# Optimization experiments

Measured on AMD Instinct MI355X. Metric: run time of the kernel, lower is better.

Reference implementation:

```python
import jax, jax.numpy as jnp
import numpy as np

PS = 32    # base patch size
SUB = 16   # subdivided patch size produced by sigmoid_round for up-weighted patches


def _sigmoid_round_np(x):
    # mirrors torch: round(32*sigmoid(x-24) + 16*(1-sigmoid(x-24)))
    s = 1.0 / (1.0 + np.exp(-(x - 24.0)))
    return np.round(32.0 * s + 16.0 * (1.0 - s)).astype(np.int64)


def _build_importance(P):
    # deterministic importance weights: even patches slightly above the mean
    # (-> adaptive size 16, subdivided), odd patches below (-> size 32, kept).
    avg = 1.0 / P
    a = avg * (2.0 ** (1.0 / 12.0)) * 1.001
    b = 2.0 * avg - a
    iw = np.empty(P, np.float64)
    iw[0::2] = a
    iw[1::2] = b
    return iw


def _build_token_index(P, G):
    # Reproduces the torch module's per-patch structural decision at trace time
    # (numpy on deterministic constants -> static shapes, jit-safe).
    iw = _build_importance(P)
    avg = iw.mean()
    sizes = _sigmoid_round_np(PS * (avg ** 12) / (iw ** 12))
    tok = []
    for i in range(P):
        r, c = i // G, i % G
        if 7 < sizes[i] < PS:  # subdivided into (PS/SUB)^2 = 4 sub-patches, row-major
            for dr in range(PS // SUB):
                for dc in range(PS // SUB):
                    tok.append(G * G + (2 * r + dr) * (2 * G) + (2 * c + dc))
        else:                   # full 32x32 patch token
            tok.append(r * G + c)
    return np.asarray(tok, np.int32)


def setup_inputs() -> dict:
    key = jax.random.key(0)
    k1, k2, k3 = jax.random.split(key, 3)
    B, C, H, E = 32, 3, 512, 768
    x = jax.random.normal(k1, (B, C, H, H), jnp.float32)
    patch_weight = jax.random.normal(k2, (E, C, PS, PS), jnp.float32) * 0.02
    patch_bias = jax.random.normal(k3, (E,), jnp.float32) * 0.02
    P = (H // PS) ** 2
    importance_w = jnp.asarray(_build_importance(P), jnp.float32)
    return {"x": x, "importance_w": importance_w, "patch_weight": patch_weight,
            "patch_bias": patch_bias, "num_patches": P}


def reference(x, importance_w, patch_weight, patch_bias, num_patches):
    B, C, H, _ = x.shape
    E = patch_weight.shape[0]
    G = H // PS            # 32x32 patch grid side
    kd = PS // SUB         # kernel divisor = 2
    tok_idx = _build_token_index(num_patches, G)  # static gather structure

    # full-size patches: stride-PS conv on each 32x32 tile == one GEMM
    # x tiles: (b, c, r, i, q, j) with row = r*PS+i, col = q*PS+j
    full = jnp.einsum('bcriqj,ecij->brqe',
                      x.reshape(B, C, G, PS, G, PS), patch_weight) + patch_bias

    # averaged 16x16 kernel: view(E,C,kd,kd,SUB,SUB).mean(dim=2).mean(dim=2)
    w_sub = patch_weight.reshape(E, C, kd, kd, SUB, SUB).mean(axis=(2, 3))
    sub = jnp.einsum('bcriqj,ecij->brqe',
                     x.reshape(B, C, kd * G, SUB, kd * G, SUB), w_sub) + patch_bias

    # token pool: [full 32-tiles (G*G), then all 16-tiles ((2G)^2)]; gather in
    # original patch order with subdivided patches expanded in place.
    pool = jnp.concatenate([full.reshape(B, G * G, E),
                            sub.reshape(B, (kd * G) ** 2, E)], axis=1)
    return pool[:, tok_idx, :]
```

## Files before the change

### kernel.cpp

```cpp
#include <hip/hip_runtime.h>
#include <stdint.h>


typedef __attribute__((ext_vector_type(8))) short bf16x8;
typedef __attribute__((ext_vector_type(8))) unsigned short ushort8;
typedef __attribute__((ext_vector_type(4))) float f32x4;

__device__ __forceinline__ unsigned short f2bf(float f) {
  union { float f; unsigned u; } v; v.f = f;
  return (unsigned short)((v.u + 0x7fffu + ((v.u >> 16) & 1u)) >> 16);
}
__device__ __forceinline__ float bf2f(unsigned short h) {
  union { unsigned u; float f; } v; v.u = ((unsigned)h) << 16; return v.f;
}

__global__ __launch_bounds__(256) void prep_w(const float* __restrict__ pw,
                                              unsigned short* __restrict__ Wf,
                                              unsigned short* __restrict__ Ws) {
  int bid = blockIdx.x, t = threadIdx.x;
  if (bid < 2304) {
    int g = bid * 256 + t;
    float4 v = ((const float4*)pw)[g];
    ((ushort4*)Wf)[g] = make_ushort4(f2bf(v.x), f2bf(v.y), f2bf(v.z), f2bf(v.w));
  } else {
    int g = (bid - 2304) * 256 + t;
    int e = g / 192;
    int rem = g - e * 192;
    int cc = rem >> 6, r2 = rem & 63, s = r2 >> 2, t4 = r2 & 3;
    const float* base = pw + ((size_t)((e * 3 + cc) * 32 + (s >> 1)) * 32
                              + 16 * (s & 1) + 4 * t4);
    float4 q0 = *(const float4*)(base);
    float4 q1 = *(const float4*)(base + 8 * 32);
    float4 q2 = *(const float4*)(base + 16 * 32);
    float4 q3 = *(const float4*)(base + 24 * 32);
    ((ushort4*)Ws)[g] = make_ushort4(
        f2bf(0.25f * (q0.x + q1.x + q2.x + q3.x)),
        f2bf(0.25f * (q0.y + q1.y + q2.y + q3.y)),
        f2bf(0.25f * (q0.z + q1.z + q2.z + q3.z)),
        f2bf(0.25f * (q0.w + q1.w + q2.w + q3.w)));
  }
}

__global__ __launch_bounds__(256) void gemm_fused(
    const float* __restrict__ x,
    const unsigned short* __restrict__ Wf, const unsigned short* __restrict__ Ws,
    const float* __restrict__ bias, unsigned short* __restrict__ Pf,
    float* __restrict__ out) {
  __shared__ unsigned short Asm[128 * 64];
  __shared__ unsigned short Bsm[128 * 64];

  int bid = (blockIdx.x & 7) * 192 + (blockIdx.x >> 3);

  const unsigned short* Bbase;
  int rsB, bm, bn, kofs, which, kc = 0;
  int ccsh, iish, iimask, jjmask;
  if (bid < 768) {
    which = 0;
    int grp = bid / 6; bn = bid - grp * 6;
    bm = grp >> 2; kc = grp & 3;
    rsB = 3072; kofs = kc * 768;
    Bbase = Wf;
    ccsh = 10; iish = 5; iimask = 31; jjmask = 31;
  } else {
    which = 1;
    int id = bid - 768;
    bm = id / 6; bn = id - bm * 6;
    rsB = 768; kofs = 0;
    Bbase = Ws;
    ccsh = 8; iish = 4; iimask = 15; jjmask = 15;
  }

  int t = threadIdx.x;
  int lane = t & 63;
  int wv = t >> 6, wr = wv >> 1, wc = wv & 1;
  int lr = lane & 15, lk = lane >> 4;

  int kbase = kofs + (t & 7) * 8;
  int abase[4];
#pragma unroll
  for (int is = 0; is < 4; ++is) {
    int m = bm * 128 + (t >> 3) + is * 32;
    int b, r, cp, extra;
    if (which == 0) {
      b = m >> 7; int p = m & 127; int i = 2 * p + 1;
      r = i >> 4; cp = i & 15; extra = 0;
    } else {
      b = m >> 9; int q = m & 511; int p = q >> 2, s = q & 3;
      int dr = s >> 1, dc = s & 1; int i = 2 * p;
      r = i >> 4; cp = i & 15; extra = dr * 8192 + dc * 16;
    }
    abase[is] = b * 786432 + r * 16384 + cp * 32 + extra;
  }
  const unsigned short* b_src = Bbase + (size_t)(bn * 128 + (t >> 3)) * rsB
                                + (t & 7) * 8 + kofs;
  unsigned short* as_dst = &Asm[t * 8];
  unsigned short* bs_dst = &Bsm[t * 8];

  f32x4 acc[4][4];
#pragma unroll
  for (int mm = 0; mm < 4; ++mm)
#pragma unroll
    for (int nn = 0; nn < 4; ++nn) acc[mm][nn] = (f32x4){0.f, 0.f, 0.f, 0.f};

  for (int k0 = 0; k0 < 768; k0 += 64) {
#pragma unroll
    for (int is = 0; is < 4; ++is)
      __builtin_amdgcn_global_load_lds(
          (const __attribute__((address_space(1))) void*)(b_src + (size_t)is * 32 * rsB + k0),
          (__attribute__((address_space(3))) void*)(bs_dst + is * 2048), 16, 0, 0);
    float4 va[4][2];
    int k = kbase + k0;
    int koff = (k >> ccsh) * 262144 + ((k >> iish) & iimask) * 512 + (k & jjmask);
#pragma unroll
    for (int is = 0; is < 4; ++is) {
      const float4* s4 = (const float4*)(x + abase[is] + koff);
      va[is][0] = s4[0]; va[is][1] = s4[1];
    }
#pragma unroll
    for (int is = 0; is < 4; ++is) {
      ushort8 v;
      v[0] = f2bf(va[is][0].x); v[1] = f2bf(va[is][0].y);
      v[2] = f2bf(va[is][0].z); v[3] = f2bf(va[is][0].w);
      v[4] = f2bf(va[is][1].x); v[5] = f2bf(va[is][1].y);
      v[6] = f2bf(va[is][1].z); v[7] = f2bf(va[is][1].w);
      *(ushort8*)(as_dst + is * 2048) = v;
    }
    __syncthreads();
#pragma unroll
    for (int kk = 0; kk < 64; kk += 32) {
      bf16x8 af[4], bf[4];
#pragma unroll
      for (int mm = 0; mm < 4; ++mm)
        af[mm] = *(const bf16x8*)&Asm[(wr * 64 + mm * 16 + lr) * 64 + kk + lk * 8];
#pragma unroll
      for (int nn = 0; nn < 4; ++nn)
        bf[nn] = *(const bf16x8*)&Bsm[(wc * 64 + nn * 16 + lr) * 64 + kk + lk * 8];
#pragma unroll
      for (int mm = 0; mm < 4; ++mm)
#pragma unroll
        for (int nn = 0; nn < 4; ++nn)
          acc[mm][nn] = __builtin_amdgcn_mfma_f32_16x16x32_bf16(af[mm], bf[nn], acc[mm][nn], 0, 0, 0);
    }
    __syncthreads();
  }

#pragma unroll
  for (int mm = 0; mm < 4; ++mm) {
    int trow = wr * 64 + mm * 16 + lk * 4;
#pragma unroll
    for (int reg = 0; reg < 4; ++reg) {
      int grow = bm * 128 + trow + reg;
      if (which == 0) {
        unsigned short* pdst = Pf + ((size_t)(kc * 4096 + grow)) * 768;
#pragma unroll
        for (int nn = 0; nn < 4; ++nn) {
          int gcol = bn * 128 + wc * 64 + nn * 16 + lr;
          pdst[gcol] = f2bf(acc[mm][nn][reg]);
        }
      } else {
        int b = grow >> 9, tt2 = grow & 511, p = tt2 >> 2, s = tt2 & 3;
        size_t obase = (size_t)(b * 640 + 5 * p + s) * 768;
#pragma unroll
        for (int nn = 0; nn < 4; ++nn) {
          int gcol = bn * 128 + wc * 64 + nn * 16 + lr;
          out[obase + gcol] = acc[mm][nn][reg] + bias[gcol];
        }
      }
    }
  }
}

__global__ __launch_bounds__(256) void reduce_full(
    const unsigned short* __restrict__ Pf, const float* __restrict__ bias,
    float* __restrict__ out) {
  int q = blockIdx.x * 256 + threadIdx.x;
  int m = q / 192, c4 = q - m * 192;
  float4 sacc = ((const float4*)bias)[c4];
#pragma unroll
  for (int kc = 0; kc < 4; ++kc) {
    ushort4 u = ((const ushort4*)(Pf + ((size_t)(kc * 4096 + m)) * 768))[c4];
    sacc.x += bf2f(u.x); sacc.y += bf2f(u.y);
    sacc.z += bf2f(u.z); sacc.w += bf2f(u.w);
  }
  int b = m >> 7, p = m & 127;
  size_t obase = (size_t)(b * 640 + 5 * p + 4) * 768;
  ((float4*)(out + obase))[c4] = sacc;
}

extern "C" void kernel_launch(void* const* d_in, const int* in_sizes, int n_in,
                              void* d_out, int out_size, void* d_ws, size_t ws_size,
                              hipStream_t stream) {
  const float* x  = (const float*)d_in[0];
  const float* pw = (const float*)d_in[2];
  const float* pb = (const float*)d_in[3];
  float* out = (float*)d_out;

  unsigned short* Wf = (unsigned short*)d_ws;
  unsigned short* Ws = Wf + 2359296;
  unsigned short* Pf = Ws + 589824;

  prep_w<<<2880, 256, 0, stream>>>(pw, Wf, Ws);
  gemm_fused<<<1536, 256, 0, stream>>>(x, Wf, Ws, pb, Pf, out);
  reduce_full<<<3072, 256, 0, stream>>>(Pf, pb, out);
}
```

Before: 244.6 us.

## Double-buffer GEMM LDS tiles with BK=32, padded A and swizzled B

```diff
diff --git a/kernel.cpp b/kernel.cpp
--- a/kernel.cpp
+++ b/kernel.cpp
@@ -41,13 +41,13 @@
   }
 }
 
-__global__ __launch_bounds__(256) void gemm_fused(
+__global__ __launch_bounds__(256, 3) void gemm_fused(
     const float* __restrict__ x,
     const unsigned short* __restrict__ Wf, const unsigned short* __restrict__ Ws,
     const float* __restrict__ bias, unsigned short* __restrict__ Pf,
     float* __restrict__ out) {
-  __shared__ unsigned short Asm[128 * 64];
-  __shared__ unsigned short Bsm[128 * 64];
+  __shared__ unsigned short Asm[2][128 * 40];
+  __shared__ unsigned short Bsm[2][128 * 32];
 
   int bid = (blockIdx.x & 7) * 192 + (blockIdx.x >> 3);
 
@@ -75,26 +75,27 @@
   int wv = t >> 6, wr = wv >> 1, wc = wv & 1;
   int lr = lane & 15, lk = lane >> 4;
 
-  int kbase = kofs + (t & 7) * 8;
-  int abase[4];
-#pragma unroll
-  for (int is = 0; is < 4; ++is) {
-    int m = bm * 128 + (t >> 3) + is * 32;
+  int abase[2], kA[2], awr[2];
+  const unsigned short* bsrc[2];
+#pragma unroll
+  for (int is = 0; is < 2; ++is) {
+    int slot = t + 256 * is;
+    int row = slot >> 2, ch = slot & 3;
+    int m = bm * 128 + row;
     int b, r, cp, extra;
     if (which == 0) {
       b = m >> 7; int p = m & 127; int i = 2 * p + 1;
       r = i >> 4; cp = i & 15; extra = 0;
     } else {
-      b = m >> 9; int q = m & 511; int p = q >> 2, s = q & 3;
-      int dr = s >> 1, dc = s & 1; int i = 2 * p;
-      r = i >> 4; cp = i & 15; extra = dr * 8192 + dc * 16;
+      b = m >> 9; int q = m & 511; int p = q >> 2, sq = q & 3;
+      int i = 2 * p; r = i >> 4; cp = i & 15;
+      extra = (sq >> 1) * 8192 + (sq & 1) * 16;
     }
     abase[is] = b * 786432 + r * 16384 + cp * 32 + extra;
-  }
-  const unsigned short* b_src = Bbase + (size_t)(bn * 128 + (t >> 3)) * rsB
-                                + (t & 7) * 8 + kofs;
-  unsigned short* as_dst = &Asm[t * 8];
-  unsigned short* bs_dst = &Bsm[t * 8];
+    kA[is] = kofs + ch * 8;
+    awr[is] = row * 40 + ch * 8;
+    bsrc[is] = Bbase + (size_t)(bn * 128 + row) * rsB + kofs + ((ch ^ (row & 3)) * 8);
+  }
 
   f32x4 acc[4][4];
 #pragma unroll
@@ -102,44 +103,78 @@
 #pragma unroll
     for (int nn = 0; nn < 4; ++nn) acc[mm][nn] = (f32x4){0.f, 0.f, 0.f, 0.f};
 
-  for (int k0 = 0; k0 < 768; k0 += 64) {
-#pragma unroll
-    for (int is = 0; is < 4; ++is)
+  {
+    float4 va[2][2];
+#pragma unroll
+    for (int is = 0; is < 2; ++is)
       __builtin_amdgcn_global_load_lds(
-          (const __attribute__((address_space(1))) void*)(b_src + (size_t)is * 32 * rsB + k0),
-          (__attribute__((address_space(3))) void*)(bs_dst + is * 2048), 16, 0, 0);
-    float4 va[4][2];
-    int k = kbase + k0;
-    int koff = (k >> ccsh) * 262144 + ((k >> iish) & iimask) * 512 + (k & jjmask);
-#pragma unroll
-    for (int is = 0; is < 4; ++is) {
+          (const __attribute__((address_space(1))) void*)(bsrc[is]),
+          (__attribute__((address_space(3))) void*)(&Bsm[0][(t + 256 * is) * 8]),
+          16, 0, 0);
+#pragma unroll
+    for (int is = 0; is < 2; ++is) {
+      int kl = kA[is];
+      int koff = (kl >> ccsh) * 262144 + ((kl >> iish) & iimask) * 512 + (kl & jjmask);
       const float4* s4 = (const float4*)(x + abase[is] + koff);
       va[is][0] = s4[0]; va[is][1] = s4[1];
     }
 #pragma unroll
-    for (int is = 0; is < 4; ++is) {
+    for (int is = 0; is < 2; ++is) {
       ushort8 v;
       v[0] = f2bf(va[is][0].x); v[1] = f2bf(va[is][0].y);
       v[2] = f2bf(va[is][0].z); v[3] = f2bf(va[is][0].w);
       v[4] = f2bf(va[is][1].x); v[5] = f2bf(va[is][1].y);
       v[6] = f2bf(va[is][1].z); v[7] = f2bf(va[is][1].w);
-      *(ushort8*)(as_dst + is * 2048) = v;
+      *(ushort8*)&Asm[0][awr[is]] = v;
     }
     __syncthreads();
-#pragma unroll
-    for (int kk = 0; kk < 64; kk += 32) {
-      bf16x8 af[4], bf[4];
-#pragma unroll
-      for (int mm = 0; mm < 4; ++mm)
-        af[mm] = *(const bf16x8*)&Asm[(wr * 64 + mm * 16 + lr) * 64 + kk + lk * 8];
+  }
+
+  for (int s = 0; s < 24; ++s) {
+    int cur = s & 1, nxt = cur ^ 1;
+    float4 va[2][2];
+    if (s < 23) {
+      int k0n = (s + 1) * 32;
+#pragma unroll
+      for (int is = 0; is < 2; ++is)
+        __builtin_amdgcn_global_load_lds(
+            (const __attribute__((address_space(1))) void*)(bsrc[is] + k0n),
+            (__attribute__((address_space(3))) void*)(&Bsm[nxt][(t + 256 * is) * 8]),
+            16, 0, 0);
+#pragma unroll
+      for (int is = 0; is < 2; ++is) {
+        int kl = kA[is] + k0n;
+        int koff = (kl >> ccsh) * 262144 + ((kl >> iish) & iimask) * 512 + (kl & jjmask);
+        const float4* s4 = (const float4*)(x + abase[is] + koff);
+        va[is][0] = s4[0]; va[is][1] = s4[1];
+      }
+    }
+    bf16x8 af[4], bfr[4];
+#pragma unroll
+    for (int mm = 0; mm < 4; ++mm) {
+      int rowA = wr * 64 + mm * 16 + lr;
+      af[mm] = *(const bf16x8*)&Asm[cur][rowA * 40 + lk * 8];
+    }
+#pragma unroll
+    for (int nn = 0; nn < 4; ++nn) {
+      int rowB = wc * 64 + nn * 16 + lr;
+      bfr[nn] = *(const bf16x8*)&Bsm[cur][rowB * 32 + ((lk ^ (lr & 3)) * 8)];
+    }
+#pragma unroll
+    for (int mm = 0; mm < 4; ++mm)
 #pragma unroll
       for (int nn = 0; nn < 4; ++nn)
-        bf[nn] = *(const bf16x8*)&Bsm[(wc * 64 + nn * 16 + lr) * 64 + kk + lk * 8];
-#pragma unroll
-      for (int mm = 0; mm < 4; ++mm)
-#pragma unroll
-        for (int nn = 0; nn < 4; ++nn)
-          acc[mm][nn] = __builtin_amdgcn_mfma_f32_16x16x32_bf16(af[mm], bf[nn], acc[mm][nn], 0, 0, 0);
+        acc[mm][nn] = __builtin_amdgcn_mfma_f32_16x16x32_bf16(af[mm], bfr[nn], acc[mm][nn], 0, 0, 0);
+    if (s < 23) {
+#pragma unroll
+      for (int is = 0; is < 2; ++is) {
+        ushort8 v;
+        v[0] = f2bf(va[is][0].x); v[1] = f2bf(va[is][0].y);
+        v[2] = f2bf(va[is][0].z); v[3] = f2bf(va[is][0].w);
+        v[4] = f2bf(va[is][1].x); v[5] = f2bf(va[is][1].y);
+        v[6] = f2bf(va[is][1].z); v[7] = f2bf(va[is][1].w);
+        *(ushort8*)&Asm[nxt][awr[is]] = v;
+      }
     }
     __syncthreads();
   }
@@ -158,8 +193,8 @@
           pdst[gcol] = f2bf(acc[mm][nn][reg]);
         }
       } else {
-        int b = grow >> 9, tt2 = grow & 511, p = tt2 >> 2, s = tt2 & 3;
-        size_t obase = (size_t)(b * 640 + 5 * p + s) * 768;
+        int b = grow >> 9, tt2 = grow & 511, p = tt2 >> 2, sq = tt2 & 3;
+        size_t obase = (size_t)(b * 640 + 5 * p + sq) * 768;
 #pragma unroll
         for (int nn = 0; nn < 4; ++nn) {
           int gcol = bn * 128 + wc * 64 + nn * 16 + lr;
```

New measurement: 246.1 us. Within noise of the previous version (+0.6%).
